# Optimization experiments

Hardware: AMD Instinct MI355X
Metric: run time of the kernel (lower is better)

Reference implementation:

```python
import jax, jax.numpy as jnp
import numpy as np

N = 512
IN_F = 128
OUT_F = 64
H = 4
NEG_INF = -9000000000000000.0


def setup_inputs() -> dict:
    key = jax.random.key(0)
    k = jax.random.split(key, 7)
    scale = 0.1
    return {
        "h": jax.random.normal(k[0], (N, IN_F), dtype=jnp.float32),
        "adj": jax.random.randint(k[1], (N, N), 0, 2, dtype=jnp.int32),
        "edge_weights": jax.random.uniform(k[2], (N, N), dtype=jnp.float32),
        "W": jax.random.normal(k[3], (H * OUT_F, IN_F), dtype=jnp.float32) * scale,
        "a": jax.random.normal(k[4], (H, 2 * OUT_F), dtype=jnp.float32) * scale,
        "U": jax.random.normal(k[5], (H * OUT_F, IN_F), dtype=jnp.float32) * scale,
        "V": jax.random.normal(k[6], (H * OUT_F, H * OUT_F), dtype=jnp.float32) * scale,
    }


def reference(h, adj, edge_weights, W, a, U, V):
    n = h.shape[0]
    # h_trans: [N, H, F]
    h_trans = (h @ W.T).reshape(n, H, OUT_F)
    # Faithful replication of torch repeat+view (note: this view scrambles
    # head indices in the original code; tile+reshape is bit-identical).
    part1 = jnp.tile(h_trans, (1, 1, n)).reshape(n * n, H, OUT_F)
    part2 = jnp.tile(h_trans, (n, 1, 1))  # already [N*N, H, F]
    a_input = jnp.concatenate([part1, part2], axis=2)  # [N*N, H, 2F]
    e_raw = (a_input * a[None, :, :]).sum(axis=2).reshape(n, n, H)
    e_raw = jax.nn.leaky_relu(e_raw, negative_slope=0.2)
    e_mod = e_raw * edge_weights[:, :, None]
    attention = jnp.where(adj[:, :, None] > 0, e_mod, NEG_INF)
    alpha = jax.nn.softmax(attention, axis=1)  # softmax over neighbors j
    # per-head aggregation: c[i,h,f] = sum_j alpha[i,j,h] * h_trans[j,h,f]
    c_virtual = jnp.einsum('ijh,jhf->ihf', alpha, h_trans).reshape(n, H * OUT_F)
    return jax.nn.sigmoid(h @ U.T + c_virtual @ V.T)
```

## Files before the change

### kernel.cpp

```cpp
#include <hip/hip_runtime.h>
#include <math.h>


typedef short short8 __attribute__((ext_vector_type(8)));
typedef float f32x4 __attribute__((ext_vector_type(4)));
union CDu { f32x4 v; float f[4]; };

#define MFMA(A,B,C) __builtin_amdgcn_mfma_f32_16x16x32_bf16((A),(B),(C),0,0,0)

__device__ __forceinline__ unsigned pk2(float lo, float hi) {
    return __builtin_amdgcn_perm(__float_as_uint(hi) + 0x8000u,
                                 __float_as_uint(lo) + 0x8000u, 0x07060302u);
}
__device__ __forceinline__ float asf(unsigned u) { return __uint_as_float(u); }

__global__ __launch_bounds__(256) void k1(
    const float* __restrict__ h, const float* __restrict__ W,
    const float* __restrict__ a, const float* __restrict__ U,
    const float* __restrict__ V,
    ushort* __restrict__ htbT, float* __restrict__ s1, float* __restrict__ s2p,
    unsigned* __restrict__ Ub, unsigned* __restrict__ Vb)
{
    const int t = threadIdx.x;
    if (blockIdx.x >= 256) {
        const int m = (blockIdx.x - 256) * 256 + t;
        const float2* U2 = (const float2*)U;
        const float2* V2 = (const float2*)V;
        #pragma unroll
        for (int k = 0; k < 2; ++k) {
            float2 f = U2[m + k * 8192];
            Ub[m + k * 8192] = pk2(f.x, f.y);
        }
        #pragma unroll
        for (int k = 0; k < 4; ++k) {
            float2 f = V2[m + k * 8192];
            Vb[m + k * 8192] = pk2(f.x, f.y);
        }
        return;
    }
    __shared__ float hsh[2 * 128];
    __shared__ float ash[512];
    __shared__ float hts[2 * 256];
    const int i0 = blockIdx.x * 2;
    if (t < 64)       ((float4*)hsh)[t]      = ((const float4*)(h + i0 * 128))[t];
    else if (t < 192) ((float4*)ash)[t - 64] = ((const float4*)a)[t - 64];
    __syncthreads();

    float acc0 = 0.f, acc1 = 0.f;
    const float4* Wv = (const float4*)(W + t * 128);
    #pragma unroll
    for (int kk = 0; kk < 32; ++kk) {
        float4 w4 = Wv[kk];
        const float* h0 = hsh + kk * 4;
        const float* h1 = hsh + 128 + kk * 4;
        acc0 += w4.x * h0[0] + w4.y * h0[1] + w4.z * h0[2] + w4.w * h0[3];
        acc1 += w4.x * h1[0] + w4.y * h1[1] + w4.z * h1[2] + w4.w * h1[3];
    }
    *(unsigned*)((char*)htbT + t * 1024 + i0 * 2) = pk2(acc0, acc1);
    hts[t]       = acc0;
    hts[256 + t] = acc1;
    __syncthreads();

    if (t < 40) {
        const int rr = t & 1, o = t >> 1;
        const float* x;
        const float* y;
        if (o < 16) { x = hts + rr * 256 + (o >> 2) * 64;  y = ash + (o & 3) * 128; }
        else        { x = hts + rr * 256 + (o - 16) * 64;  y = ash + (o - 16) * 128 + 64; }
        float s = 0.f;
        #pragma unroll
        for (int ff = 0; ff < 64; ++ff) {
            int f = (ff + (t << 3)) & 63;
            s += x[f] * y[f];
        }
        if (o < 16) s1[(i0 + rr) * 16 + (o >> 2) * 4 + (o & 3)] = s;
        else        s2p[(o - 16) * 512 + i0 + rr] = s;
    }
}

__global__ __launch_bounds__(512) void k2(
    const int* __restrict__ adj, const float* __restrict__ ew,
    const ushort* __restrict__ htbT, const float* __restrict__ s1,
    const float* __restrict__ s2p,
    float* __restrict__ nump, float* __restrict__ denp)
{
    __shared__ __align__(16) char hTl[256 * 272];
    __shared__ __align__(16) char Es[32 * 272];
    __shared__ float s2sh[512];
    __shared__ float s1sh[128];
    const int t = threadIdx.x, l = t & 63, w = t >> 6;
    const int it = blockIdx.x >> 2, q = blockIdx.x & 3;
    const int i0 = it * 8, jg = q * 128;

    #pragma unroll
    for (int p = 0; p < 8; ++p) {
        int lin = p * 512 + t, row = lin >> 4, jseg = (lin & 15) * 8;
        uint4 v = *(const uint4*)(htbT + row * 512 + jg + jseg);
        *(uint4*)(hTl + row * 272 + jseg * 2) = v;
    }
    s2sh[t] = s2p[(t >> 7) * 512 + jg + (t & 127)];
    if (t < 128) s1sh[t] = s1[(i0 + (t >> 4)) * 16 + (t & 15)];
    __syncthreads();

    {
        const int rh = t >> 4, j8 = (t & 15) * 8;
        const int r = rh & 7, hh = rh >> 3;
        const float s1v = s1sh[r * 16 + q * 4 + hh];
        const int base = (i0 + r) * 512 + jg + j8;
        int4   a0 = *(const int4*)(adj + base), a1 = *(const int4*)(adj + base + 4);
        float4 w0 = *(const float4*)(ew + base), w1 = *(const float4*)(ew + base + 4);
        float v[8];
        const float* sp = s2sh + hh * 128 + j8;
        int   ai[8] = {a0.x,a0.y,a0.z,a0.w,a1.x,a1.y,a1.z,a1.w};
        float wi[8] = {w0.x,w0.y,w0.z,w0.w,w1.x,w1.y,w1.z,w1.w};
        float den = 0.f;
        #pragma unroll
        for (int k = 0; k < 8; ++k) {
            float e = s1v + sp[k];
            e = (e >= 0.f) ? e : 0.2f * e;
            e = (ai[k] > 0) ? e * wi[k] : -9.0e15f;
            v[k] = __expf(e);
            den += v[k];
        }
        *(uint4*)(Es + rh * 272 + j8 * 2) =
            make_uint4(pk2(v[0],v[1]), pk2(v[2],v[3]), pk2(v[4],v[5]), pk2(v[6],v[7]));
        #pragma unroll
        for (int o = 1; o < 16; o <<= 1) den += __shfl_xor(den, o, 64);
        if ((l & 15) == 0) denp[(q * 64 + it) * 32 + rh] = den;
    }
    __syncthreads();

    {
        #pragma unroll
        for (int pp = 0; pp < 2; ++pp) {
            const int p = w * 2 + pp, mt = p >> 3, ntl = p & 7;
            const int nt = mt * 8 + ntl;
            f32x4 acc = {0.f, 0.f, 0.f, 0.f};
            #pragma unroll
            for (int ks = 0; ks < 4; ++ks) {
                const int kb = ks * 32 + (l >> 4) * 8;
                short8 Af = *(const short8*)(Es + (mt * 16 + (l & 15)) * 272 + kb * 2);
                short8 Bf = *(const short8*)(hTl + (nt * 16 + (l & 15)) * 272 + kb * 2);
                acc = MFMA(Af, Bf, acc);
            }
            CDu cd; cd.v = acc;
            const int fcol = ntl * 16 + (l & 15);
            const int fh = fcol >> 6;
            #pragma unroll
            for (int q4 = 0; q4 < 4; ++q4) {
                const int rloc = (l >> 4) * 4 + q4;
                if ((rloc >> 3) == fh) {
                    const int rh = mt * 16 + rloc;
                    nump[((q * 64 + it) * 32 + rh) * 64 + (fcol & 63)] = cd.f[q4];
                }
            }
        }
    }
}

__global__ __launch_bounds__(512) void k3(
    const float* __restrict__ h, const float* __restrict__ nump,
    const float* __restrict__ denp, const unsigned* __restrict__ Ub,
    const unsigned* __restrict__ Vb, float* __restrict__ out)
{
    __shared__ float hsh[2 * 128];
    __shared__ float csh[2 * 256];
    __shared__ float psum[4 * 256];
    const int t = threadIdx.x;
    const int i0 = blockIdx.x * 2;
    const int it = i0 >> 3, rbase = i0 & 7;

    if (t < 64) ((float4*)hsh)[t] = ((const float4*)(h + i0 * 128))[t];
    {
        const int r = t >> 8, hf = t & 255, hh = hf >> 6, fp = hf & 63;
        const int rh = hh * 8 + rbase + r;
        float num = 0.f, den = 0.f;
        #pragma unroll
        for (int qq = 0; qq < 4; ++qq) {
            num += nump[((qq * 64 + it) * 32 + rh) * 64 + fp];
            den += denp[(qq * 64 + it) * 32 + rh];
        }
        csh[r * 256 + hf] = num / den;
    }
    __syncthreads();

    {
        const int half = t >> 8, col = t & 255;
        float acc0 = 0.f, acc1 = 0.f;
        const uint4* Up = (const uint4*)(Ub + col * 64 + half * 32);
        #pragma unroll
        for (int b4 = 0; b4 < 8; ++b4) {
            uint4 uv = Up[b4];
            unsigned ua[4] = {uv.x, uv.y, uv.z, uv.w};
            #pragma unroll
            for (int e = 0; e < 4; ++e) {
                const int k = half * 64 + b4 * 8 + e * 2;
                float ulo = asf(ua[e] << 16), uhi = asf(ua[e] & 0xffff0000u);
                acc0 += ulo * hsh[k]       + uhi * hsh[k + 1];
                acc1 += ulo * hsh[128 + k] + uhi * hsh[128 + k + 1];
            }
        }
        const uint4* Vp = (const uint4*)(Vb + col * 128 + half * 64);
        #pragma unroll
        for (int b4 = 0; b4 < 16; ++b4) {
            uint4 vv = Vp[b4];
            unsigned va[4] = {vv.x, vv.y, vv.z, vv.w};
            #pragma unroll
            for (int e = 0; e < 4; ++e) {
                const int k = half * 128 + b4 * 8 + e * 2;
                float vlo = asf(va[e] << 16), vhi = asf(va[e] & 0xffff0000u);
                acc0 += vlo * csh[k]       + vhi * csh[k + 1];
                acc1 += vlo * csh[256 + k] + vhi * csh[256 + k + 1];
            }
        }
        psum[(half * 2 + 0) * 256 + col] = acc0;
        psum[(half * 2 + 1) * 256 + col] = acc1;
    }
    __syncthreads();
    {
        const int r = t >> 8, col = t & 255;
        float x = psum[r * 256 + col] + psum[(2 + r) * 256 + col];
        out[(i0 + r) * 256 + col] = 1.f / (1.f + __expf(-x));
    }
}

extern "C" void kernel_launch(void* const* d_in, const int* in_sizes, int n_in,
                              void* d_out, int out_size, void* d_ws, size_t ws_size,
                              hipStream_t stream) {
    const float* h   = (const float*)d_in[0];
    const int*   adj = (const int*)d_in[1];
    const float* ew  = (const float*)d_in[2];
    const float* W   = (const float*)d_in[3];
    const float* a   = (const float*)d_in[4];
    const float* U   = (const float*)d_in[5];
    const float* V   = (const float*)d_in[6];
    float* out = (float*)d_out;

    ushort*  htbT = (ushort*)d_ws;
    float*   s1   = (float*)(htbT + 256 * 512);
    float*   s2p  = s1 + 512 * 16;
    unsigned* Ub  = (unsigned*)(s2p + 2048);
    unsigned* Vb  = Ub + 16384;
    float*   nump = (float*)(Vb + 32768);
    float*   denp = nump + 4 * 64 * 32 * 64;

    k1<<<288, 256, 0, stream>>>(h, W, a, U, V, htbT, s1, s2p, Ub, Vb);
    k2<<<256, 512, 0, stream>>>(adj, ew, htbT, s1, s2p, nump, denp);
    k3<<<256, 512, 0, stream>>>(h, nump, denp, Ub, Vb, out);
}
```

Before: 25.03 us.

## Fuse attention aggregation and output projection into one kernel per 8-row tile

Merges k2 and k3 into a single 1024-thread kernel that handles 8 rows across all 512 neighbors. The softmax numerator and denominator now stay in shared memory, so the partial-sum workspace round trip and one launch go away. The B operand is now read straight from global memory instead of being staged in LDS. The trade is a grid of only 64 blocks on a GPU with many more CUs, which may leave the device underused and lengthen the serial work inside each block.

```diff
diff --git a/kernel.cpp b/kernel.cpp
--- a/kernel.cpp
+++ b/kernel.cpp
@@ -78,149 +78,137 @@
     }
 }
 
-__global__ __launch_bounds__(512) void k2(
-    const int* __restrict__ adj, const float* __restrict__ ew,
-    const ushort* __restrict__ htbT, const float* __restrict__ s1,
-    const float* __restrict__ s2p,
-    float* __restrict__ nump, float* __restrict__ denp)
+__global__ __launch_bounds__(1024) void k2(
+    const float* __restrict__ h, const int* __restrict__ adj,
+    const float* __restrict__ ew, const ushort* __restrict__ htbT,
+    const float* __restrict__ s1, const float* __restrict__ s2p,
+    const unsigned* __restrict__ Ub, const unsigned* __restrict__ Vb,
+    float* __restrict__ out)
 {
-    __shared__ __align__(16) char hTl[256 * 272];
-    __shared__ __align__(16) char Es[32 * 272];
-    __shared__ float s2sh[512];
+    __shared__ float s2sh[4 * 512];
+    __shared__ float hshK[8 * 128];
     __shared__ float s1sh[128];
+    __shared__ __align__(16) char Es[32 * 1040];
+    __shared__ float numsh[32 * 68];
+    __shared__ float csh[8 * 256];
+    __shared__ float psum[4 * 2048];
+    __shared__ float den_s[32], dinv[32];
+
     const int t = threadIdx.x, l = t & 63, w = t >> 6;
-    const int it = blockIdx.x >> 2, q = blockIdx.x & 3;
-    const int i0 = it * 8, jg = q * 128;
+    const int i0 = blockIdx.x * 8;
+
+    if (t < 512)      ((float4*)s2sh)[t]       = ((const float4*)s2p)[t];
+    else if (t < 768) ((float4*)hshK)[t - 512] = ((const float4*)(h + i0 * 128))[t - 512];
+    else if (t < 896) s1sh[t - 768] = s1[(i0 + ((t - 768) >> 4)) * 16 + ((t - 768) & 15)];
+    __syncthreads();
+
+    {
+        const int rh = t >> 5, jseg = (t & 31) * 16;
+        const int r = rh & 7, hh = rh >> 3;
+        const float s1v = s1sh[r * 16 + (jseg >> 7) * 4 + hh];
+        const int base = (i0 + r) * 512 + jseg;
+        float den = 0.f;
+        float v[16];
+        #pragma unroll
+        for (int q = 0; q < 4; ++q) {
+            int4   av = *(const int4*)  (adj + base + q * 4);
+            float4 wv = *(const float4*)(ew  + base + q * 4);
+            const float* sp = s2sh + hh * 512 + jseg + q * 4;
+            int   ai[4] = {av.x, av.y, av.z, av.w};
+            float wi[4] = {wv.x, wv.y, wv.z, wv.w};
+            #pragma unroll
+            for (int k = 0; k < 4; ++k) {
+                float e = s1v + sp[k];
+                e = (e >= 0.f) ? e : 0.2f * e;
+                e = (ai[k] > 0) ? e * wi[k] : -9.0e15f;
+                float x = __expf(e);
+                v[q * 4 + k] = x; den += x;
+            }
+        }
+        *(uint4*)(Es + rh * 1040 + jseg * 2) =
+            make_uint4(pk2(v[0],v[1]), pk2(v[2],v[3]), pk2(v[4],v[5]), pk2(v[6],v[7]));
+        *(uint4*)(Es + rh * 1040 + jseg * 2 + 16) =
+            make_uint4(pk2(v[8],v[9]), pk2(v[10],v[11]), pk2(v[12],v[13]), pk2(v[14],v[15]));
+        #pragma unroll
+        for (int o = 16; o; o >>= 1) den += __shfl_xor(den, o, 64);
+        if ((l & 31) == 0) den_s[rh] = den;
+    }
+    __syncthreads();
+    if (t < 32) dinv[t] = 1.f / den_s[t];
+
+    {
+        const int mt = w >> 3;
+        const ushort* gB = htbT + (w * 16 + (l & 15)) * 512 + (l >> 4) * 8;
+        const char* aRow = Es + (mt * 16 + (l & 15)) * 1040 + (l >> 4) * 16;
+        f32x4 acc = {0.f, 0.f, 0.f, 0.f};
+        #pragma unroll
+        for (int ks = 0; ks < 16; ++ks) {
+            short8 Af = *(const short8*)(aRow + ks * 64);
+            short8 Bf = *(const short8*)(gB + ks * 32);
+            acc = MFMA(Af, Bf, acc);
+        }
+        CDu cd; cd.v = acc;
+        const int sel = (w >> 2) & 1;
+        #pragma unroll
+        for (int q = 0; q < 4; ++q) {
+            int rloc = (l >> 4) * 4 + q;
+            if ((rloc >> 3) == sel)
+                numsh[(mt * 16 + rloc) * 68 + (w & 3) * 16 + (l & 15)] = cd.f[q];
+        }
+    }
+    __syncthreads();
 
     #pragma unroll
-    for (int p = 0; p < 8; ++p) {
-        int lin = p * 512 + t, row = lin >> 4, jseg = (lin & 15) * 8;
-        uint4 v = *(const uint4*)(htbT + row * 512 + jg + jseg);
-        *(uint4*)(hTl + row * 272 + jseg * 2) = v;
-    }
-    s2sh[t] = s2p[(t >> 7) * 512 + jg + (t & 127)];
-    if (t < 128) s1sh[t] = s1[(i0 + (t >> 4)) * 16 + (t & 15)];
+    for (int p = 0; p < 2; ++p) {
+        int idx = p * 1024 + t, r = idx >> 8, hf = idx & 255;
+        int rh = (hf >> 6) * 8 + r;
+        csh[idx] = numsh[rh * 68 + (hf & 63)] * dinv[rh];
+    }
     __syncthreads();
 
     {
-        const int rh = t >> 4, j8 = (t & 15) * 8;
-        const int r = rh & 7, hh = rh >> 3;
-        const float s1v = s1sh[r * 16 + q * 4 + hh];
-        const int base = (i0 + r) * 512 + jg + j8;
-        int4   a0 = *(const int4*)(adj + base), a1 = *(const int4*)(adj + base + 4);
-        float4 w0 = *(const float4*)(ew + base), w1 = *(const float4*)(ew + base + 4);
-        float v[8];
-        const float* sp = s2sh + hh * 128 + j8;
-        int   ai[8] = {a0.x,a0.y,a0.z,a0.w,a1.x,a1.y,a1.z,a1.w};
-        float wi[8] = {w0.x,w0.y,w0.z,w0.w,w1.x,w1.y,w1.z,w1.w};
-        float den = 0.f;
-        #pragma unroll
-        for (int k = 0; k < 8; ++k) {
-            float e = s1v + sp[k];
-            e = (e >= 0.f) ? e : 0.2f * e;
-            e = (ai[k] > 0) ? e * wi[k] : -9.0e15f;
-            v[k] = __expf(e);
-            den += v[k];
-        }
-        *(uint4*)(Es + rh * 272 + j8 * 2) =
-            make_uint4(pk2(v[0],v[1]), pk2(v[2],v[3]), pk2(v[4],v[5]), pk2(v[6],v[7]));
-        #pragma unroll
-        for (int o = 1; o < 16; o <<= 1) den += __shfl_xor(den, o, 64);
-        if ((l & 15) == 0) denp[(q * 64 + it) * 32 + rh] = den;
-    }
-    __syncthreads();
-
-    {
-        #pragma unroll
-        for (int pp = 0; pp < 2; ++pp) {
-            const int p = w * 2 + pp, mt = p >> 3, ntl = p & 7;
-            const int nt = mt * 8 + ntl;
-            f32x4 acc = {0.f, 0.f, 0.f, 0.f};
+        const int col = t & 255, grp = t >> 8;
+        float acc[8] = {0.f,0.f,0.f,0.f,0.f,0.f,0.f,0.f};
+        if (grp < 2) {
+            const uint4* Up = (const uint4*)(Ub + col * 64 + grp * 32);
             #pragma unroll
-            for (int ks = 0; ks < 4; ++ks) {
-                const int kb = ks * 32 + (l >> 4) * 8;
-                short8 Af = *(const short8*)(Es + (mt * 16 + (l & 15)) * 272 + kb * 2);
-                short8 Bf = *(const short8*)(hTl + (nt * 16 + (l & 15)) * 272 + kb * 2);
-                acc = MFMA(Af, Bf, acc);
-            }
-            CDu cd; cd.v = acc;
-            const int fcol = ntl * 16 + (l & 15);
-            const int fh = fcol >> 6;
-            #pragma unroll
-            for (int q4 = 0; q4 < 4; ++q4) {
-                const int rloc = (l >> 4) * 4 + q4;
-                if ((rloc >> 3) == fh) {
-                    const int rh = mt * 16 + rloc;
-                    nump[((q * 64 + it) * 32 + rh) * 64 + (fcol & 63)] = cd.f[q4];
+            for (int b4 = 0; b4 < 8; ++b4) {
+                uint4 uv = Up[b4];
+                unsigned ua[4] = {uv.x, uv.y, uv.z, uv.w};
+                #pragma unroll
+                for (int e = 0; e < 4; ++e) {
+                    int k = grp * 64 + b4 * 8 + e * 2;
+                    float lo = asf(ua[e] << 16), hi = asf(ua[e] & 0xffff0000u);
+                    #pragma unroll
+                    for (int r = 0; r < 8; ++r)
+                        acc[r] += lo * hshK[r * 128 + k] + hi * hshK[r * 128 + k + 1];
                 }
             }
-        }
-    }
-}
-
-__global__ __launch_bounds__(512) void k3(
-    const float* __restrict__ h, const float* __restrict__ nump,
-    const float* __restrict__ denp, const unsigned* __restrict__ Ub,
-    const unsigned* __restrict__ Vb, float* __restrict__ out)
-{
-    __shared__ float hsh[2 * 128];
-    __shared__ float csh[2 * 256];
-    __shared__ float psum[4 * 256];
-    const int t = threadIdx.x;
-    const int i0 = blockIdx.x * 2;
-    const int it = i0 >> 3, rbase = i0 & 7;
-
-    if (t < 64) ((float4*)hsh)[t] = ((const float4*)(h + i0 * 128))[t];
-    {
-        const int r = t >> 8, hf = t & 255, hh = hf >> 6, fp = hf & 63;
-        const int rh = hh * 8 + rbase + r;
-        float num = 0.f, den = 0.f;
-        #pragma unroll
-        for (int qq = 0; qq < 4; ++qq) {
-            num += nump[((qq * 64 + it) * 32 + rh) * 64 + fp];
-            den += denp[(qq * 64 + it) * 32 + rh];
-        }
-        csh[r * 256 + hf] = num / den;
-    }
-    __syncthreads();
-
-    {
-        const int half = t >> 8, col = t & 255;
-        float acc0 = 0.f, acc1 = 0.f;
-        const uint4* Up = (const uint4*)(Ub + col * 64 + half * 32);
-        #pragma unroll
-        for (int b4 = 0; b4 < 8; ++b4) {
-            uint4 uv = Up[b4];
-            unsigned ua[4] = {uv.x, uv.y, uv.z, uv.w};
+        } else {
+            const uint4* Vp = (const uint4*)(Vb + col * 128 + (grp - 2) * 64);
             #pragma unroll
-            for (int e = 0; e < 4; ++e) {
-                const int k = half * 64 + b4 * 8 + e * 2;
-                float ulo = asf(ua[e] << 16), uhi = asf(ua[e] & 0xffff0000u);
-                acc0 += ulo * hsh[k]       + uhi * hsh[k + 1];
-                acc1 += ulo * hsh[128 + k] + uhi * hsh[128 + k + 1];
+            for (int b4 = 0; b4 < 16; ++b4) {
+                uint4 vv = Vp[b4];
+                unsigned va[4] = {vv.x, vv.y, vv.z, vv.w};
+                #pragma unroll
+                for (int e = 0; e < 4; ++e) {
+                    int k = (grp - 2) * 128 + b4 * 8 + e * 2;
+                    float lo = asf(va[e] << 16), hi = asf(va[e] & 0xffff0000u);
+                    #pragma unroll
+                    for (int r = 0; r < 8; ++r)
+                        acc[r] += lo * csh[r * 256 + k] + hi * csh[r * 256 + k + 1];
+                }
             }
         }
-        const uint4* Vp = (const uint4*)(Vb + col * 128 + half * 64);
-        #pragma unroll
-        for (int b4 = 0; b4 < 16; ++b4) {
-            uint4 vv = Vp[b4];
-            unsigned va[4] = {vv.x, vv.y, vv.z, vv.w};
-            #pragma unroll
-            for (int e = 0; e < 4; ++e) {
-                const int k = half * 128 + b4 * 8 + e * 2;
-                float vlo = asf(va[e] << 16), vhi = asf(va[e] & 0xffff0000u);
-                acc0 += vlo * csh[k]       + vhi * csh[k + 1];
-                acc1 += vlo * csh[256 + k] + vhi * csh[256 + k + 1];
-            }
-        }
-        psum[(half * 2 + 0) * 256 + col] = acc0;
-        psum[(half * 2 + 1) * 256 + col] = acc1;
-    }
-    __syncthreads();
-    {
-        const int r = t >> 8, col = t & 255;
-        float x = psum[r * 256 + col] + psum[(2 + r) * 256 + col];
-        out[(i0 + r) * 256 + col] = 1.f / (1.f + __expf(-x));
+        #pragma unroll
+        for (int r = 0; r < 8; ++r) psum[grp * 2048 + r * 256 + col] = acc[r];
+    }
+    __syncthreads();
+    #pragma unroll
+    for (int p = 0; p < 2; ++p) {
+        int idx = p * 1024 + t;
+        float x = psum[idx] + psum[2048 + idx] + psum[4096 + idx] + psum[6144 + idx];
+        out[i0 * 256 + idx] = 1.f / (1.f + __expf(-x));
     }
 }
 
@@ -241,10 +229,7 @@
     float*   s2p  = s1 + 512 * 16;
     unsigned* Ub  = (unsigned*)(s2p + 2048);
     unsigned* Vb  = Ub + 16384;
-    float*   nump = (float*)(Vb + 32768);
-    float*   denp = nump + 4 * 64 * 32 * 64;
 
     k1<<<288, 256, 0, stream>>>(h, W, a, U, V, htbT, s1, s2p, Ub, Vb);
-    k2<<<256, 512, 0, stream>>>(adj, ew, htbT, s1, s2p, nump, denp);
-    k3<<<256, 512, 0, stream>>>(h, nump, denp, Ub, Vb, out);
-}
+    k2<<<64, 1024, 0, stream>>>(h, adj, ew, htbT, s1, s2p, Ub, Vb, out);
+}
```

Result: slower. 35.76 us (+42.9%).
